# Performance work log

Measured on AMD Instinct MI355X. Metric: run time of the kernel, lower is better.

The kernel has to match this reference:

```python
import jax, jax.numpy as jnp
import numpy as np

EPS = 1e-5
N_HEAD = 8

def setup_inputs() -> dict:
    key = jax.random.key(0)
    ks = jax.random.split(key, 8)
    n, c, h, w = 8, 512, 64, 64
    feats_in = 512
    x = jax.random.normal(ks[0], (n, c, h, w), jnp.float32)
    cond = jax.random.normal(ks[1], (n, feats_in), jnp.float32)
    # AdaGN linear: feats_in -> 2*c
    W_ada = jax.random.normal(ks[2], (feats_in, 2 * c), jnp.float32) * (1.0 / np.sqrt(feats_in))
    b_ada = jnp.zeros((2 * c,), jnp.float32)
    # qkv 1x1 conv: c -> 3c
    W_qkv = jax.random.normal(ks[3], (3 * c, c), jnp.float32) * (1.0 / np.sqrt(c))
    b_qkv = jnp.zeros((3 * c,), jnp.float32)
    # out 1x1 conv: c -> c
    W_out = jax.random.normal(ks[4], (c, c), jnp.float32) * (1.0 / np.sqrt(c))
    b_out = jnp.zeros((c,), jnp.float32)
    return {"x": x, "cond": cond, "W_ada": W_ada, "b_ada": b_ada,
            "W_qkv": W_qkv, "b_qkv": b_qkv, "W_out": W_out, "b_out": b_out}

def reference(x, cond, W_ada, b_ada, W_qkv, b_qkv, W_out, b_out):
    n, c, h, w = x.shape
    nh = N_HEAD
    dh = c // nh
    s = h * w
    # AdaGN: GroupNorm with 1 group, no affine, then scale/shift from cond
    scales_shifts = cond @ W_ada + b_ada  # [n, 2c]
    scales, shifts = scales_shifts[:, :c], scales_shifts[:, c:]
    xf = x.reshape(n, -1)
    mean = xf.mean(axis=1, keepdims=True)
    var = xf.var(axis=1, keepdims=True)
    normed = ((xf - mean) * jax.lax.rsqrt(var + EPS)).reshape(n, c, h, w)
    normed = shifts[:, :, None, None] + normed * (scales[:, :, None, None] + 1.0)
    # qkv 1x1 conv
    qkv = jnp.einsum('nchw,oc->nohw', normed, W_qkv) + b_qkv[None, :, None, None]
    # view [n, nh*3, dh, s] then transpose -> [n, nh*3, s, dh]
    qkv = qkv.reshape(n, nh * 3, dh, s).transpose(0, 1, 3, 2)
    q, k, v = jnp.split(qkv, 3, axis=1)  # each [n, nh, s, dh]
    scale = dh ** (-0.25)
    att = jnp.einsum('nhsd,nhtd->nhst', q * scale, k * scale)
    att = jax.nn.softmax(att, axis=-1)
    y = jnp.einsum('nhst,nhtd->nhsd', att, v)  # [n, nh, s, dh]
    y = y.transpose(0, 1, 3, 2).reshape(n, c, h, w)
    out = jnp.einsum('nchw,oc->nohw', y, W_out) + b_out[None, :, None, None]
    return x + out
```

## Files before the change

### kernel.cpp

```cpp
#include <hip/hip_runtime.h>

#define NB   8
#define CC   512
#define SS   4096
#define NHD  8
#define DH   64
#define FEAT 512
#define NPER (CC*SS)

typedef unsigned short ushort_t;
typedef __attribute__((ext_vector_type(8))) short bf16x8;
typedef __attribute__((ext_vector_type(4))) float f32x4;

__device__ inline float b2f(ushort_t h) {
    union { unsigned int u; float f; } v; v.u = ((unsigned int)h) << 16; return v.f;
}
__device__ inline ushort_t f2b(float f) {
    union { float f; unsigned int u; } v; v.f = f;
    unsigned int u = v.u;
    u += 0x7fffu + ((u >> 16) & 1u);
    return (ushort_t)(u >> 16);
}
__device__ inline void unpack8(uint4 v, ushort_t* us) {
    us[0] = v.x & 0xffff; us[1] = v.x >> 16;
    us[2] = v.y & 0xffff; us[3] = v.y >> 16;
    us[4] = v.z & 0xffff; us[5] = v.z >> 16;
    us[6] = v.w & 0xffff; us[7] = v.w >> 16;
}
__device__ inline float loadIn(const void* p, size_t idx, int isf) {
    return isf ? ((const float*)p)[idx] : b2f(((const ushort_t*)p)[idx]);
}
__device__ inline void load8(const void* p, size_t idx, int isf, float* f) {
    if (isf) {
        const float* q = (const float*)p + idx;
        float4 a = *(const float4*)q, b = *(const float4*)(q + 4);
        f[0]=a.x; f[1]=a.y; f[2]=a.z; f[3]=a.w; f[4]=b.x; f[5]=b.y; f[6]=b.z; f[7]=b.w;
    } else {
        uint4 v = *(const uint4*)((const ushort_t*)p + idx);
        ushort_t us[8]; unpack8(v, us);
        for (int j = 0; j < 8; ++j) f[j] = b2f(us[j]);
    }
}
__device__ inline bf16x8 loadfrag(const void* p, size_t idx, int isf) {
    if (isf) {
        float f[8]; load8(p, idx, 1, f);
        bf16x8 r;
        for (int j = 0; j < 8; ++j) r[j] = (short)f2b(f[j]);
        return r;
    }
    union { uint4 u; bf16x8 v; } cvt;
    cvt.u = *(const uint4*)((const ushort_t*)p + idx);
    return cvt.v;
}

__global__ void probe_kernel(const unsigned int* __restrict__ x, int* __restrict__ flag) {
    unsigned int w = x[threadIdx.x & 63];
    unsigned int elo = (w >> 7) & 0xFF;
    int hit = (elo >= 0x60 && elo <= 0x9F) ? 1 : 0;
    for (int m = 1; m < 64; m <<= 1) hit += __shfl_xor(hit, m, 64);
    if (threadIdx.x == 0) *flag = (hit >= 40) ? 0 : 1;
}

__global__ __launch_bounds__(256) void ada_kernel(
    const void* __restrict__ cond, const void* __restrict__ W,
    const void* __restrict__ bias, float* __restrict__ out,
    const int* __restrict__ flagp)
{
    int isf = *flagp;
    int n = blockIdx.x;
    int j = blockIdx.y * 256 + threadIdx.x;
    float acc = loadIn(bias, j, isf);
    for (int k = 0; k < FEAT; ++k)
        acc += loadIn(cond, (size_t)n * FEAT + k, isf) * loadIn(W, (size_t)k * (2 * CC) + j, isf);
    out[n * (2 * CC) + j] = acc;
}

__global__ __launch_bounds__(256) void stats_kernel(
    const void* __restrict__ x, float* __restrict__ part, const int* __restrict__ flagp)
{
    int isf = *flagp;
    int n = blockIdx.x, blk = blockIdx.y;
    int tid = threadIdx.x;
    float s = 0.f, ss = 0.f;
    size_t base8 = (size_t)blk * 4096 + tid;
    for (int i = 0; i < 16; ++i) {
        float f[8];
        load8(x, ((size_t)n * NPER) + (base8 + (size_t)i * 256) * 8, isf, f);
        for (int j = 0; j < 8; ++j) { s += f[j]; ss += f[j] * f[j]; }
    }
    for (int m = 1; m < 64; m <<= 1) { s += __shfl_xor(s, m, 64); ss += __shfl_xor(ss, m, 64); }
    int w = tid >> 6;
    if ((tid & 63) == 0) {
        part[(size_t)n * 512 + (blk * 4 + w) * 2 + 0] = s;
        part[(size_t)n * 512 + (blk * 4 + w) * 2 + 1] = ss;
    }
}

__global__ __launch_bounds__(256) void coef_kernel(
    const float* __restrict__ ada, const float* __restrict__ part,
    float* __restrict__ coefA, float* __restrict__ coefB)
{
    __shared__ float reds[4], redss[4], mv[2];
    int n = blockIdx.x;
    int tid = threadIdx.x;
    float s  = part[(size_t)n * 512 + tid * 2 + 0];
    float ss = part[(size_t)n * 512 + tid * 2 + 1];
    for (int m = 1; m < 64; m <<= 1) { s += __shfl_xor(s, m, 64); ss += __shfl_xor(ss, m, 64); }
    int w = tid >> 6, lane = tid & 63;
    if (lane == 0) { reds[w] = s; redss[w] = ss; }
    __syncthreads();
    if (tid == 0) {
        float S  = (reds[0] + reds[1]) + (reds[2] + reds[3]);
        float S2 = (redss[0] + redss[1]) + (redss[2] + redss[3]);
        float inv = 1.f / (float)NPER;
        float mean = S * inv;
        float var  = S2 * inv - mean * mean;
        mv[0] = mean;
        mv[1] = rsqrtf(var + 1e-5f);
    }
    __syncthreads();
    float mean = mv[0], r = mv[1];
    int c = blockIdx.y * 256 + tid;
    float a = (ada[n * (2 * CC) + c] + 1.f) * r;
    coefA[n * CC + c] = a;
    coefB[n * CC + c] = ada[n * (2 * CC) + CC + c] - mean * a;
}

__global__ __launch_bounds__(256) void qkv_gemm_kernel(
    const void* __restrict__ A, const void* __restrict__ X, const void* __restrict__ bias,
    ushort_t* __restrict__ C,
    const float* __restrict__ coefA, const float* __restrict__ coefB,
    const int* __restrict__ flagp, int nb, int hb, int hc)
{
    __shared__ __align__(16) short Alds[64][72];
    __shared__ __align__(16) short Blds[64][72];
    int isf = *flagp;
    int z = blockIdx.z;
    int nIdx = nb + z;
    int yb = blockIdx.y;
    int p = yb / hc, hh = yb % hc;
    int arow0 = p * 512 + (hb + hh) * 64;
    size_t cbase = ((size_t)(z * 3 + p) * (hc * 64) + hh * 64) * SS;
    int n0 = blockIdx.x * 64;
    int tid = threadIdx.x;
    int w = tid >> 6, lane = tid & 63;
    int quad = lane >> 4, l16 = lane & 15;
    int wm = (w >> 1) * 32, wn = (w & 1) * 32;
    f32x4 acc[2][2] = {};

    for (int k0 = 0; k0 < 512; k0 += 64) {
        __syncthreads();
        for (int it = 0; it < 2; ++it) {
            int chunk = tid + it * 256;
            int row = chunk >> 3, cb = chunk & 7;
            float f[8];
            load8(A, (size_t)(arow0 + row) * 512 + k0 + cb * 8, isf, f);
            short o[8];
            for (int j = 0; j < 8; ++j) o[j] = (short)f2b(f[j]);
            *(uint4*)&Alds[row][cb * 8] = *(uint4*)o;
        }
        for (int it = 0; it < 2; ++it) {
            int chunk = tid + it * 256;
            int c = chunk >> 3, hb8 = chunk & 7;
            int ch = k0 + c;
            float f[8];
            load8(X, (size_t)nIdx * NPER + (size_t)ch * SS + n0 + hb8 * 8, isf, f);
            float a = coefA[nIdx * CC + ch], b = coefB[nIdx * CC + ch];
            for (int j = 0; j < 8; ++j)
                Blds[hb8 * 8 + j][c] = (short)f2b(a * f[j] + b);
        }
        __syncthreads();
        for (int kk = 0; kk < 2; ++kk) {
            bf16x8 af[2], bfv[2];
            for (int mi = 0; mi < 2; ++mi)
                af[mi] = *(const bf16x8*)&Alds[wm + mi * 16 + l16][kk * 32 + quad * 8];
            for (int ni = 0; ni < 2; ++ni)
                bfv[ni] = *(const bf16x8*)&Blds[wn + ni * 16 + l16][kk * 32 + quad * 8];
            for (int mi = 0; mi < 2; ++mi)
                for (int ni = 0; ni < 2; ++ni)
                    acc[mi][ni] = __builtin_amdgcn_mfma_f32_16x16x32_bf16(
                        af[mi], bfv[ni], acc[mi][ni], 0, 0, 0);
        }
    }
    if (p < 2) {
        const float SCL = 0.42467078f;
        for (int mi = 0; mi < 2; ++mi)
            for (int ni = 0; ni < 2; ++ni) {
                int col = n0 + wn + ni * 16 + l16;
                int d0 = wm + mi * 16 + quad * 4;
                ushort_t pk[4];
                for (int r = 0; r < 4; ++r) {
                    float v = (acc[mi][ni][r] + loadIn(bias, arow0 + d0 + r, isf)) * SCL;
                    pk[r] = f2b(v);
                }
                *(ushort4*)&C[cbase + (size_t)col * 64 + d0] =
                    make_ushort4(pk[0], pk[1], pk[2], pk[3]);
            }
    } else {
        for (int mi = 0; mi < 2; ++mi)
            for (int ni = 0; ni < 2; ++ni) {
                int col = n0 + wn + ni * 16 + l16;
                for (int r = 0; r < 4; ++r) {
                    int rowl = wm + mi * 16 + quad * 4 + r;
                    float v = acc[mi][ni][r] + loadIn(bias, arow0 + rowl, isf);
                    C[cbase + (size_t)rowl * SS + col] = f2b(v);
                }
            }
    }
}

__global__ __launch_bounds__(256, 4) void attn_kernel(
    const ushort_t* __restrict__ qkv,
    ushort_t* __restrict__ y,
    int nb, int hb, int hc)
{
    __shared__ __align__(16) short Klds[64][64];
    __shared__ __align__(16) short Vlds[64][64];

    int s0 = blockIdx.x * 128;
    int hl = blockIdx.y;
    int z = blockIdx.z;
    int n = nb + z;
    int hcc = hc * 64;
    const ushort_t* Q = qkv + ((size_t)(z * 3 + 0) * hcc + hl * 64) * SS;
    const ushort_t* K = qkv + ((size_t)(z * 3 + 1) * hcc + hl * 64) * SS;
    const ushort_t* V = qkv + ((size_t)(z * 3 + 2) * hcc + hl * 64) * SS;

    int tid = threadIdx.x;
    int w = tid >> 6, lane = tid & 63;
    int quad = lane >> 4, l16 = lane & 15;
    int sw = l16 & 7;

    bf16x8 qf[2][2];
    for (int si = 0; si < 2; ++si)
        for (int kk = 0; kk < 2; ++kk)
            qf[si][kk] = *(const bf16x8*)&Q[(size_t)(s0 + w * 32 + si * 16 + l16) * 64
                                            + kk * 32 + quad * 8];

    const short ONE = 0x3F80;
    bf16x8 ones = { ONE, ONE, ONE, ONE, ONE, ONE, ONE, ONE };

    f32x4 o[2][4] = {};
    f32x4 sum_acc[2] = {};

    for (int t0 = 0; t0 < SS; t0 += 64) {
        __syncthreads();
        for (int it = 0; it < 2; ++it) {
            int chunk = tid + it * 256;
            int row = chunk >> 3, cb = chunk & 7;
            int cw = (cb ^ (row & 7)) * 8;
            *(uint4*)&Klds[row][cw] = *(const uint4*)&K[(size_t)(t0 + row) * 64 + cb * 8];
            *(uint4*)&Vlds[row][cw] = *(const uint4*)&V[(size_t)row * SS + t0 + cb * 8];
        }
        __syncthreads();

        for (int kk = 0; kk < 2; ++kk) {
            f32x4 sv[2][2];
            for (int ntl = 0; ntl < 2; ++ntl) {
                int nt = kk * 2 + ntl;
                bf16x8 kf0 = *(const bf16x8*)&Klds[nt * 16 + l16][((0 * 4 + quad) ^ sw) * 8];
                bf16x8 kf1 = *(const bf16x8*)&Klds[nt * 16 + l16][((1 * 4 + quad) ^ sw) * 8];
                for (int si = 0; si < 2; ++si) {
                    f32x4 a = { -16.f, -16.f, -16.f, -16.f };
                    a = __builtin_amdgcn_mfma_f32_16x16x32_bf16(kf0, qf[si][0], a, 0, 0, 0);
                    a = __builtin_amdgcn_mfma_f32_16x16x32_bf16(kf1, qf[si][1], a, 0, 0, 0);
                    sv[ntl][si] = a;
                }
            }

            bf16x8 vf[4];
            for (int dt = 0; dt < 4; ++dt)
                vf[dt] = *(const bf16x8*)&Vlds[dt * 16 + l16][((kk * 4 + quad) ^ sw) * 8];

            for (int si = 0; si < 2; ++si) {
                float p0 = exp2f(sv[0][si][0]), p1 = exp2f(sv[0][si][1]);
                float p2 = exp2f(sv[0][si][2]), p3 = exp2f(sv[0][si][3]);
                float p4 = exp2f(sv[1][si][0]), p5 = exp2f(sv[1][si][1]);
                float p6 = exp2f(sv[1][si][2]), p7 = exp2f(sv[1][si][3]);
                unsigned int x0, x1, y0, y1;
                asm("v_cvt_pk_bf16_f32 %0, %1, %2" : "=v"(x0) : "v"(p0), "v"(p1));
                asm("v_cvt_pk_bf16_f32 %0, %1, %2" : "=v"(x1) : "v"(p2), "v"(p3));
                asm("v_cvt_pk_bf16_f32 %0, %1, %2" : "=v"(y0) : "v"(p4), "v"(p5));
                asm("v_cvt_pk_bf16_f32 %0, %1, %2" : "=v"(y1) : "v"(p6), "v"(p7));
                asm("v_permlane32_swap_b32 %0, %1" : "+v"(x0), "+v"(y0));
                asm("v_permlane32_swap_b32 %0, %1" : "+v"(x1), "+v"(y1));
                asm("v_permlane16_swap_b32 %0, %1" : "+v"(x0), "+v"(y0));
                asm("v_permlane16_swap_b32 %0, %1" : "+v"(x1), "+v"(y1));
                union { unsigned int u[4]; bf16x8 v; } frag;
                frag.u[0] = x0; frag.u[1] = x1; frag.u[2] = y0; frag.u[3] = y1;

                sum_acc[si] = __builtin_amdgcn_mfma_f32_16x16x32_bf16(frag.v, ones, sum_acc[si], 0, 0, 0);
                for (int dt = 0; dt < 4; ++dt)
                    o[si][dt] = __builtin_amdgcn_mfma_f32_16x16x32_bf16(frag.v, vf[dt], o[si][dt], 0, 0, 0);
            }
        }
    }

    for (int si = 0; si < 2; ++si) {
        f32x4 inv;
        for (int r = 0; r < 4; ++r) inv[r] = 1.0f / sum_acc[si][r];
        for (int dt = 0; dt < 4; ++dt) {
            int d = dt * 16 + l16;
            int cidx = (hb + hl) * DH + d;
            size_t bidx = ((size_t)n * CC + cidx) * SS + s0 + w * 32 + si * 16 + quad * 4;
            ushort_t pk[4];
            for (int r = 0; r < 4; ++r) pk[r] = f2b(o[si][dt][r] * inv[r]);
            *(ushort4*)&y[bidx] = make_ushort4(pk[0], pk[1], pk[2], pk[3]);
        }
    }
}

__global__ __launch_bounds__(512) void out_gemm_kernel(
    const void* __restrict__ W, const void* __restrict__ bias, const void* __restrict__ x,
    const ushort_t* __restrict__ ybuf, float* __restrict__ out,
    const int* __restrict__ flagp)
{
    __shared__ __align__(16) short Ylds[64][264];
    int isf = *flagp;
    int n = blockIdx.y;
    int s0 = blockIdx.x * 64;
    int tid = threadIdx.x;
    int w = tid >> 6, lane = tid & 63;
    int quad = lane >> 4, l16 = lane & 15;
    const ushort_t* Yb = ybuf + (size_t)n * ((size_t)CC * SS);
    float* Op = out + (size_t)n * NPER;

    f32x4 acc[4][4] = {};
    for (int kh = 0; kh < 2; ++kh) {
        __syncthreads();
        int ch = (tid & 255) + kh * 256;
        int cg = tid >> 8;
        for (int cb = 0; cb < 4; ++cb) {
            uint4 v = *(const uint4*)&Yb[(size_t)ch * SS + s0 + cg * 32 + cb * 8];
            ushort_t us[8]; unpack8(v, us);
            for (int j = 0; j < 8; ++j) Ylds[cg * 32 + cb * 8 + j][tid & 255] = (short)us[j];
        }
        __syncthreads();
        for (int k0 = 0; k0 < 256; k0 += 32) {
            bf16x8 af[4];
            for (int mi = 0; mi < 4; ++mi)
                af[mi] = loadfrag(W, (size_t)(w * 64 + mi * 16 + l16) * 512 + kh * 256 + k0 + quad * 8, isf);
            for (int ni = 0; ni < 4; ++ni) {
                bf16x8 bfv = *(const bf16x8*)&Ylds[ni * 16 + l16][k0 + quad * 8];
                for (int mi = 0; mi < 4; ++mi)
                    acc[mi][ni] = __builtin_amdgcn_mfma_f32_16x16x32_bf16(
                        af[mi], bfv, acc[mi][ni], 0, 0, 0);
            }
        }
    }

    for (int mi = 0; mi < 4; ++mi)
        for (int ni = 0; ni < 4; ++ni) {
            int col = s0 + ni * 16 + l16;
            for (int r = 0; r < 4; ++r) {
                int m = w * 64 + mi * 16 + quad * 4 + r;
                size_t idx = (size_t)m * SS + col;
                float v = acc[mi][ni][r] + loadIn(bias, m, isf)
                        + loadIn(x, (size_t)n * NPER + idx, isf);
                Op[idx] = v;
            }
        }
}

extern "C" void kernel_launch(void* const* d_in, const int* in_sizes, int n_in,
                              void* d_out, int out_size, void* d_ws, size_t ws_size,
                              hipStream_t stream) {
    (void)in_sizes; (void)n_in; (void)out_size;
    const void* x     = d_in[0];
    const void* cond  = d_in[1];
    const void* W_ada = d_in[2];
    const void* b_ada = d_in[3];
    const void* W_qkv = d_in[4];
    const void* b_qkv = d_in[5];
    const void* W_out = d_in[6];
    const void* b_out = d_in[7];
    float* out = (float*)d_out;

    char* ws = (char*)d_ws;
    float* part  = (float*)ws;
    float* ada   = (float*)(ws + 16384);
    float* coefA = (float*)(ws + 49152);
    float* coefB = (float*)(ws + 65536);
    int*   flag  = (int*)(ws + 81920);
    ushort_t* ybuf   = (ushort_t*)(ws + 82176);
    const size_t BASE = 82176ULL + (size_t)NB * NPER * 2;
    ushort_t* qkvbuf = (ushort_t*)(ws + BASE);

    const size_t PER_HS = (size_t)3 * 64 * SS * 2;
    size_t avail = ws_size > BASE ? ws_size - BASE : 0;
    int NC = 1, HC = 1;
    if      (avail >= 64 * PER_HS) { NC = 8; HC = 8; }
    else if (avail >= 32 * PER_HS) { NC = 4; HC = 8; }
    else if (avail >= 16 * PER_HS) { NC = 2; HC = 8; }
    else if (avail >=  8 * PER_HS) { NC = 1; HC = 8; }
    else if (avail >=  4 * PER_HS) { NC = 1; HC = 4; }
    else if (avail >=  2 * PER_HS) { NC = 1; HC = 2; }

    probe_kernel<<<1, 64, 0, stream>>>((const unsigned int*)x, flag);
    ada_kernel  <<<dim3(NB, 4),  256, 0, stream>>>(cond, W_ada, b_ada, ada, flag);
    stats_kernel<<<dim3(NB, 64), 256, 0, stream>>>(x, part, flag);
    coef_kernel <<<dim3(NB, 2),  256, 0, stream>>>(ada, part, coefA, coefB);

    for (int nb = 0; nb < NB; nb += NC)
        for (int hb = 0; hb < NHD; hb += HC) {
            qkv_gemm_kernel<<<dim3(64, 3 * HC, NC), 256, 0, stream>>>(
                W_qkv, x, b_qkv, qkvbuf, coefA, coefB, flag, nb, hb, HC);
            attn_kernel<<<dim3(32, HC, NC), 256, 0, stream>>>(
                qkvbuf, ybuf, nb, hb, HC);
        }

    out_gemm_kernel<<<dim3(64, NB), 512, 0, stream>>>(W_out, b_out, x, ybuf, out, flag);
}
```

Before: 927.6 us.

## Double-buffer attention K/V tiles with async global-to-LDS loads

The attention kernel now keeps two LDS buffers for the K and V tiles. The next tile is prefetched with global_load_lds (direct global-to-LDS DMA) while the current tile is being computed, which drops one barrier per iteration. The XOR swizzle moves from the LDS write address to the global read address, so the LDS layout stays the same. This doubles LDS use per block, which may lower occupancy, and correctness relies on the compiler placing the vmcnt waits properly before the barrier.

Result: no change. 916.8 us (-1.2%).

```diff
diff --git a/kernel.cpp b/kernel.cpp
--- a/kernel.cpp
+++ b/kernel.cpp
@@ -51,6 +51,12 @@
     union { uint4 u; bf16x8 v; } cvt;
     cvt.u = *(const uint4*)((const ushort_t*)p + idx);
     return cvt.v;
+}
+
+typedef __attribute__((address_space(1))) const unsigned int gas_u32;
+typedef __attribute__((address_space(3))) unsigned int las_u32;
+__device__ inline void gload_lds16(const void* g, void* l) {
+    __builtin_amdgcn_global_load_lds((gas_u32*)g, (las_u32*)l, 16, 0, 0);
 }
 
 __global__ void probe_kernel(const unsigned int* __restrict__ x, int* __restrict__ flag) {
@@ -214,8 +220,8 @@
     ushort_t* __restrict__ y,
     int nb, int hb, int hc)
 {
-    __shared__ __align__(16) short Klds[64][64];
-    __shared__ __align__(16) short Vlds[64][64];
+    __shared__ __align__(16) short Klds[2][64][64];
+    __shared__ __align__(16) short Vlds[2][64][64];
 
     int s0 = blockIdx.x * 128;
     int hl = blockIdx.y;
@@ -237,29 +243,37 @@
             qf[si][kk] = *(const bf16x8*)&Q[(size_t)(s0 + w * 32 + si * 16 + l16) * 64
                                             + kk * 32 + quad * 8];
 
+    auto stage = [&](int b, int tt) {
+        #pragma unroll
+        for (int it = 0; it < 2; ++it) {
+            int chunk = it * 256 + tid;
+            int row = chunk >> 3;
+            int ssl = (chunk & 7) ^ (row & 7);
+            int cb0 = it * 256 + w * 64;
+            gload_lds16(&K[(size_t)(tt + row) * 64 + ssl * 8], (short*)Klds[b] + cb0 * 8);
+            gload_lds16(&V[(size_t)row * SS + tt + ssl * 8],   (short*)Vlds[b] + cb0 * 8);
+        }
+    };
+
     const short ONE = 0x3F80;
     bf16x8 ones = { ONE, ONE, ONE, ONE, ONE, ONE, ONE, ONE };
 
     f32x4 o[2][4] = {};
     f32x4 sum_acc[2] = {};
 
+    stage(0, 0);
+
     for (int t0 = 0; t0 < SS; t0 += 64) {
+        int cur = (t0 >> 6) & 1;
         __syncthreads();
-        for (int it = 0; it < 2; ++it) {
-            int chunk = tid + it * 256;
-            int row = chunk >> 3, cb = chunk & 7;
-            int cw = (cb ^ (row & 7)) * 8;
-            *(uint4*)&Klds[row][cw] = *(const uint4*)&K[(size_t)(t0 + row) * 64 + cb * 8];
-            *(uint4*)&Vlds[row][cw] = *(const uint4*)&V[(size_t)row * SS + t0 + cb * 8];
-        }
-        __syncthreads();
+        if (t0 + 64 < SS) stage(cur ^ 1, t0 + 64);
 
         for (int kk = 0; kk < 2; ++kk) {
             f32x4 sv[2][2];
             for (int ntl = 0; ntl < 2; ++ntl) {
                 int nt = kk * 2 + ntl;
-                bf16x8 kf0 = *(const bf16x8*)&Klds[nt * 16 + l16][((0 * 4 + quad) ^ sw) * 8];
-                bf16x8 kf1 = *(const bf16x8*)&Klds[nt * 16 + l16][((1 * 4 + quad) ^ sw) * 8];
+                bf16x8 kf0 = *(const bf16x8*)&Klds[cur][nt * 16 + l16][((0 * 4 + quad) ^ sw) * 8];
+                bf16x8 kf1 = *(const bf16x8*)&Klds[cur][nt * 16 + l16][((1 * 4 + quad) ^ sw) * 8];
                 for (int si = 0; si < 2; ++si) {
                     f32x4 a = { -16.f, -16.f, -16.f, -16.f };
                     a = __builtin_amdgcn_mfma_f32_16x16x32_bf16(kf0, qf[si][0], a, 0, 0, 0);
@@ -270,7 +284,7 @@
 
             bf16x8 vf[4];
             for (int dt = 0; dt < 4; ++dt)
-                vf[dt] = *(const bf16x8*)&Vlds[dt * 16 + l16][((kk * 4 + quad) ^ sw) * 8];
+                vf[dt] = *(const bf16x8*)&Vlds[cur][dt * 16 + l16][((kk * 4 + quad) ^ sw) * 8];
 
             for (int si = 0; si < 2; ++si) {
                 float p0 = exp2f(sv[0][si][0]), p1 = exp2f(sv[0][si][1]);
```
